# Kernel optimization log

Hardware: AMD Instinct MI355X
Metric: run time of the kernel (lower is better)

The kernel has to match this reference:

```python
import jax, jax.numpy as jnp
import numpy as np
import math

B, S = 2, 2048
DIM_MODEL = 2048
NUM_Q_HEADS = 16
GROUP_SIZE = 4
NUM_KV_HEADS = NUM_Q_HEADS // GROUP_SIZE
DIM_K = 128
RMS_EPS = 1e-6
ROPE_BASE = 10000.0


def setup_inputs() -> dict:
    key = jax.random.key(0)
    ks = jax.random.split(key, 8)
    x = jax.random.normal(ks[0], (B, S, DIM_MODEL), dtype=jnp.float32)
    mask = jnp.tril(jnp.ones((S, S), dtype=bool))  # causal
    # Linear weights stored as [in, out] so y = x @ W (bias=False everywhere)
    sd = 1.0 / math.sqrt(DIM_MODEL)
    Wq = jax.random.uniform(ks[1], (DIM_MODEL, DIM_K * NUM_Q_HEADS), jnp.float32, -sd, sd)
    Wk = jax.random.uniform(ks[2], (DIM_MODEL, DIM_K * NUM_KV_HEADS), jnp.float32, -sd, sd)
    Wv = jax.random.uniform(ks[3], (DIM_MODEL, DIM_K * NUM_KV_HEADS), jnp.float32, -sd, sd)
    sf = 1.0 / math.sqrt(DIM_K * NUM_Q_HEADS)
    Wfc = jax.random.uniform(ks[4], (DIM_K * NUM_Q_HEADS, DIM_MODEL), jnp.float32, -sf, sf)
    q_gamma = jnp.ones((DIM_K,), dtype=jnp.float32)
    k_gamma = jnp.ones((DIM_K,), dtype=jnp.float32)
    return {"x": x, "mask": mask, "Wq": Wq, "Wk": Wk, "Wv": Wv,
            "Wfc": Wfc, "q_gamma": q_gamma, "k_gamma": k_gamma}


def _rope(t):
    # t: [B, H, S, D], rotate-half RoPE
    d = t.shape[-1]
    half = d // 2
    inv_freq = 1.0 / (ROPE_BASE ** (jnp.arange(half, dtype=jnp.float32) / half))
    pos = jnp.arange(t.shape[2], dtype=jnp.float32)
    ang = pos[:, None] * inv_freq[None, :]            # [S, half]
    cos, sin = jnp.cos(ang), jnp.sin(ang)              # [S, half]
    t1, t2 = t[..., :half], t[..., half:]
    return jnp.concatenate([t1 * cos - t2 * sin, t2 * cos + t1 * sin], axis=-1)


def _rmsnorm(t, gamma):
    ms = jnp.mean(t * t, axis=-1, keepdims=True)
    return t * jax.lax.rsqrt(ms + RMS_EPS) * gamma


def reference(x, mask, Wq, Wk, Wv, Wfc, q_gamma, k_gamma):
    b, s, _ = x.shape
    q = (x @ Wq).reshape(b, s, NUM_Q_HEADS, DIM_K).transpose(0, 2, 1, 3)   # [B,Hq,S,D]
    k = (x @ Wk).reshape(b, s, NUM_KV_HEADS, DIM_K).transpose(0, 2, 1, 3)  # [B,Hkv,S,D]
    v = (x @ Wv).reshape(b, s, NUM_KV_HEADS, DIM_K).transpose(0, 2, 1, 3)
    q = _rmsnorm(_rope(q), q_gamma)
    k = _rmsnorm(_rope(k), k_gamma)
    q = q.reshape(b, NUM_KV_HEADS, GROUP_SIZE, s, DIM_K)                    # [B,Hkv,G,S,D]
    scores = jnp.einsum('bhgqd,bhkd->bhgqk', q, k) / math.sqrt(DIM_K)      # [B,Hkv,G,S,S]
    scores = jnp.where(mask, scores, -jnp.inf)
    attn = jax.nn.softmax(scores, axis=-1)  # dropout is identity in eval
    out = jnp.einsum('bhgqk,bhkd->bhgqd', attn, v)                          # [B,Hkv,G,S,D]
    out = out.reshape(b, NUM_Q_HEADS, s, DIM_K).transpose(0, 2, 1, 3)
    out = out.reshape(b, s, NUM_Q_HEADS * DIM_K) @ Wfc                      # [B,S,DM]
    return out
```

## Files before the change

kernel.cpp:

```cpp
#include <hip/hip_runtime.h>
#include <hip/hip_bf16.h>

typedef __attribute__((ext_vector_type(8))) short bf16x8;
typedef __attribute__((ext_vector_type(4))) short bf16x4;
typedef __attribute__((ext_vector_type(4))) float f32x4;

#define S_LEN 2048
#define DMODEL 2048
#define NQH 16
#define NKVH 4
#define DK 128

__device__ __forceinline__ float b2f(short u) {
  union { unsigned int i; float f; } x;
  x.i = ((unsigned int)(unsigned short)u) << 16;
  return x.f;
}
__device__ __forceinline__ short f2b(float f) {
  union { float f; unsigned int i; } x; x.f = f;
  unsigned int r = (x.i + 0x7fffu + ((x.i >> 16) & 1u)) >> 16;
  return (short)r;
}
__device__ __forceinline__ unsigned int cvtpk(float a, float b) {
  unsigned int r;
  asm("v_cvt_pk_bf16_f32 %0, %1, %2" : "=v"(r) : "v"(a), "v"(b));
  return r;
}
__device__ __forceinline__ f32x4 mfma16(bf16x8 a, bf16x8 b, f32x4 c) {
  return __builtin_amdgcn_mfma_f32_16x16x32_bf16(a, b, c, 0, 0, 0);
}
__device__ __forceinline__ void async16(short* lds, const short* g) {
  __builtin_amdgcn_global_load_lds(
      (const __attribute__((address_space(1))) unsigned int*)(const void*)g,
      (__attribute__((address_space(3))) unsigned int*)(void*)lds, 16, 0, 0);
}

__global__ void f32_to_bf16(const float* __restrict__ in, short* __restrict__ out, int n4) {
  int i = blockIdx.x * blockDim.x + threadIdx.x;
  if (i >= n4) return;
  float4 v = ((const float4*)in)[i];
  bf16x4 o;
  o[0] = f2b(v.x); o[1] = f2b(v.y); o[2] = f2b(v.z); o[3] = f2b(v.w);
  ((bf16x4*)out)[i] = o;
}

__global__ void rope_table(float* __restrict__ rt) {
  int i = blockIdx.x * blockDim.x + threadIdx.x;
  int s = i >> 6, d = i & 63;
  float ang = (float)s * __expf((float)d * -0.14391157f);
  float c, sn;
  __sincosf(ang, &sn, &c);
  rt[s * 128 + d] = c;
  rt[s * 128 + 64 + d] = sn;
}

__global__ void transpose_f2b(const float* __restrict__ in, short* __restrict__ out,
                              int R, int C) {
  __shared__ short t[32][33];
  int c0 = blockIdx.x * 32, r0 = blockIdx.y * 32;
  int tx = threadIdx.x, ty = threadIdx.y;
#pragma unroll
  for (int i = 0; i < 32; i += 8)
    t[ty + i][tx] = f2b(in[(size_t)(r0 + ty + i) * C + c0 + tx]);
  __syncthreads();
#pragma unroll
  for (int i = 0; i < 32; i += 8)
    out[(size_t)(c0 + ty + i) * R + r0 + tx] = t[tx][ty + i];
}

template <int NT, int VW>
__device__ __forceinline__ void kcore256(const short* __restrict__ Ab,
                                         const short* __restrict__ Bb,
                                         short* sm, f32x4 (&acc)[8][NT], int tid) {
  const int K = 2048;
  const int lane = tid & 63, w = tid >> 6;
  const int wm2 = w >> 2, wn4 = w & 3;
  const int l15 = lane & 15, lg = lane >> 4;
  constexpr int ABUF = 8192;
  constexpr int BBUF = NT * 2048;
  constexpr int BUFSZ = ABUF + BBUF;

  const int sr = lane >> 2, sc = lane & 3;
  const int ar0 = w * 16 + sr, ar1 = ar0 + 128;
  const short* gA0 = Ab + (size_t)ar0 * K + ((sc ^ (ar0 & 3)) * 8);
  const short* gA1 = Ab + (size_t)ar1 * K + ((sc ^ (ar1 & 3)) * 8);
  const short* gB0 = Bb + (size_t)ar0 * K + ((sc ^ (ar0 & 3)) * 8);
  const short* gB1 = Bb + (size_t)ar1 * K + ((sc ^ (ar1 & 3)) * 8);
  const int dA0 = (w * 16) * 32, dA1 = dA0 + 128 * 32;
  const int dB0 = ABUF + dA0, dB1 = ABUF + dA1;

  int aoff[8], boff[NT];
#pragma unroll
  for (int mt = 0; mt < 8; ++mt) {
    const int row = wm2 * 128 + mt * 16 + l15;
    aoff[mt] = row * 32 + ((lg * 8) ^ ((row & 3) << 3));
  }
#pragma unroll
  for (int nt = 0; nt < NT; ++nt) {
    const int row = wn4 * (NT * 16) + nt * 16 + l15;
    boff[nt] = ABUF + row * 32 + ((lg * 8) ^ ((row & 3) << 3));
  }

  auto stageA = [&](int buf, int t) {
    short* d = sm + buf * BUFSZ;
    const int o = t * 32;
    async16(d + dA0, gA0 + o);
    async16(d + dA1, gA1 + o);
  };
  auto stageB = [&](int buf, int t) {
    short* d = sm + buf * BUFSZ;
    const int o = t * 32;
    async16(d + dB0, gB0 + o);
    if constexpr (NT == 4) async16(d + dB1, gB1 + o);
  };
  auto tilebody = [&](int buf, int sbuf, int st, bool dostage) {
    const short* bc = sm + buf * BUFSZ;
    if (dostage) stageA(sbuf, st);
    bf16x8 bfr[NT], af[4];
#pragma unroll
    for (int nt = 0; nt < NT; ++nt) bfr[nt] = *(const bf16x8*)(bc + boff[nt]);
#pragma unroll
    for (int mt = 0; mt < 4; ++mt) af[mt] = *(const bf16x8*)(bc + aoff[mt]);
    __builtin_amdgcn_s_setprio(1);
#pragma unroll
    for (int mt = 0; mt < 4; ++mt)
#pragma unroll
      for (int nt = 0; nt < NT; ++nt)
        acc[mt][nt] = mfma16(af[mt], bfr[nt], acc[mt][nt]);
    __builtin_amdgcn_s_setprio(0);
    if (dostage) stageB(sbuf, st);
#pragma unroll
    for (int mt = 0; mt < 4; ++mt) af[mt] = *(const bf16x8*)(bc + aoff[4 + mt]);
    __builtin_amdgcn_s_setprio(1);
#pragma unroll
    for (int mt = 0; mt < 4; ++mt)
#pragma unroll
      for (int nt = 0; nt < NT; ++nt)
        acc[4 + mt][nt] = mfma16(af[mt], bfr[nt], acc[4 + mt][nt]);
    __builtin_amdgcn_s_setprio(0);
  };

  stageA(0, 0); stageB(0, 0);
  stageA(1, 1); stageB(1, 1);
  int cur = 0, nx2 = 2;
#pragma unroll 1
  for (int t = 0; t < 63; ++t) {
    __builtin_amdgcn_sched_barrier(0);
    if constexpr (VW == 4)
      asm volatile("s_waitcnt vmcnt(4)" ::: "memory");
    else
      asm volatile("s_waitcnt vmcnt(3)" ::: "memory");
    __builtin_amdgcn_s_barrier();
    __builtin_amdgcn_sched_barrier(0);
    tilebody(cur, nx2, t + 2, t < 62);
    cur = (cur == 2) ? 0 : cur + 1;
    nx2 = (nx2 == 2) ? 0 : nx2 + 1;
  }
  __builtin_amdgcn_sched_barrier(0);
  asm volatile("s_waitcnt vmcnt(0)" ::: "memory");
  __builtin_amdgcn_s_barrier();
  __builtin_amdgcn_sched_barrier(0);
  tilebody(cur, 0, 0, false);
}

__global__ __launch_bounds__(512) void gemm_qkv(const short* __restrict__ A,
                                                const short* __restrict__ WT,
                                                short* __restrict__ Qr,
                                                short* __restrict__ Kr,
                                                short* __restrict__ Vtr,
                                                const float* __restrict__ qg,
                                                const float* __restrict__ kg,
                                                const float* __restrict__ ropeT) {
  __shared__ __align__(16) short smem[49152];
  const int flat = blockIdx.x;
  const int xcd = flat & 7, idx = flat >> 3;
  const int mb = (xcd >> 1) * 4 + (idx & 3);
  const int nb = (xcd & 1) * 6 + (idx >> 2);
  const int tid = threadIdx.x;

  f32x4 acc[8][4] = {};
  kcore256<4, 4>(A + (size_t)mb * 256 * 2048, WT + (size_t)nb * 256 * 2048,
                 smem, acc, tid);

  const int lane = tid & 63, w = tid >> 6, wm2 = w >> 2, wn4 = w & 3;
  const int l15 = lane & 15, lg = lane >> 4;
  const int b = mb >> 3;
  short* Cs = smem;
  constexpr int CL = 264;

  for (int ph = 0; ph < 2; ++ph) {
    __syncthreads();
    if (wm2 == ph) {
#pragma unroll
      for (int mt = 0; mt < 8; ++mt)
#pragma unroll
        for (int nt = 0; nt < 4; ++nt)
#pragma unroll
          for (int rr = 0; rr < 4; ++rr)
            Cs[(mt * 16 + lg * 4 + rr) * CL + wn4 * 64 + nt * 16 + l15] =
                f2b(acc[mt][nt][rr]);
    }
    __syncthreads();
    const int srowg = mb * 256 + ph * 128;
    if (nb < 10) {
      const bool isQ = nb < 8;
      const int r = tid >> 2, quad = tid & 3;
      const int head = quad >> 1, half = quad & 1;
      const int s = (srowg + r) & 2047;
      const float* rt = ropeT + (size_t)s * 128;
      const short* crow = Cs + r * CL + head * 128;
      const float* gamma = isQ ? qg : kg;
      float ss = 0.f;
      bf16x8 ov[8];
#pragma unroll
      for (int j = 0; j < 8; ++j) {
        bf16x8 t1v = *(const bf16x8*)(crow + j * 8);
        bf16x8 t2v = *(const bf16x8*)(crow + 64 + j * 8);
        float4 c0 = *(const float4*)(rt + j * 8);
        float4 c1 = *(const float4*)(rt + j * 8 + 4);
        float4 s0 = *(const float4*)(rt + 64 + j * 8);
        float4 s1 = *(const float4*)(rt + 64 + j * 8 + 4);
        float cc[8] = {c0.x, c0.y, c0.z, c0.w, c1.x, c1.y, c1.z, c1.w};
        float sn[8] = {s0.x, s0.y, s0.z, s0.w, s1.x, s1.y, s1.z, s1.w};
#pragma unroll
        for (int i = 0; i < 8; ++i) {
          float t1 = b2f(t1v[i]), t2 = b2f(t2v[i]);
          float o = half ? (t2 * cc[i] + t1 * sn[i]) : (t1 * cc[i] - t2 * sn[i]);
          ss += o * o;
          ov[j][i] = f2b(o);
        }
      }
      ss += __shfl_xor(ss, 1);
      float inv = rsqrtf(ss * (1.0f / 128.0f) + 1e-6f);
      if (isQ) inv *= (0.08838834764831845f * 1.4426950408889634f);
      const int NH = isQ ? NQH : NKVH;
      const int hg = isQ ? (nb * 2 + head) : ((nb - 8) * 2 + head);
      short* outp = isQ ? Qr : Kr;
      short* ob = outp + ((size_t)(b * NH + hg) * S_LEN + s) * DK + half * 64;
#pragma unroll
      for (int j = 0; j < 8; ++j) {
        float4 g0 = *(const float4*)(gamma + half * 64 + j * 8);
        float4 g1 = *(const float4*)(gamma + half * 64 + j * 8 + 4);
        float gg[8] = {g0.x, g0.y, g0.z, g0.w, g1.x, g1.y, g1.z, g1.w};
        bf16x8 vv;
#pragma unroll
        for (int i = 0; i < 8; ++i) vv[i] = f2b(b2f(ov[j][i]) * inv * gg[i]);
        *(bf16x8*)(ob + j * 8) = vv;
      }
    } else {
      const int hd = tid >> 7;
      const int head = hd >> 1, sh = hd & 1;
      const int d = tid & 127;
      const int hg = (nb - 10) * 2 + head;
      const int sbase = (srowg & 2047) + sh * 64;
      short* ob = Vtr + ((size_t)(b * NKVH + hg) * DK + d) * S_LEN + sbase;
      const short* cc = Cs + head * 128 + d;
      for (int i0 = 0; i0 < 64; i0 += 8) {
        bf16x8 v;
#pragma unroll
        for (int j = 0; j < 8; ++j) {
          const int p = i0 + j;
          const int sl = sh * 64 + 16 * (p & 3) + (p >> 2);
          v[j] = cc[sl * CL];
        }
        *(bf16x8*)(ob + i0) = v;
      }
    }
  }
}

__global__ __launch_bounds__(512) void gemm_out(const short* __restrict__ A,
                                                const short* __restrict__ BT,
                                                float* __restrict__ outf) {
  __shared__ __align__(16) short smem[36864];
  const int flat = blockIdx.x;
  const int xcd = flat & 7, idx = flat >> 3;
  const int mb = (xcd >> 1) * 4 + (idx & 3);
  const int nb = (xcd & 1) * 8 + (idx >> 2);
  const int tid = threadIdx.x;

  f32x4 acc[8][2] = {};
  kcore256<2, 3>(A + (size_t)mb * 256 * 2048, BT + (size_t)nb * 128 * 2048,
                 smem, acc, tid);

  const int lane = tid & 63, w = tid >> 6, wm2 = w >> 2, wn4 = w & 3;
  const int l15 = lane & 15, lg = lane >> 4;
#pragma unroll
  for (int mt = 0; mt < 8; ++mt) {
    const int row = mb * 256 + wm2 * 128 + mt * 16 + lg * 4;
#pragma unroll
    for (int nt = 0; nt < 2; ++nt) {
      const int col = nb * 128 + wn4 * 32 + nt * 16 + l15;
#pragma unroll
      for (int r = 0; r < 4; ++r)
        outf[(size_t)(row + r) * DMODEL + col] = acc[mt][nt][r];
    }
  }
}

__device__ __forceinline__ void stage_kv(const short* __restrict__ Kb,
                                         const short* __restrict__ Vb, int kb,
                                         short* Ks, short* Vs, int w, int lane) {
#pragma unroll
  for (int i = 0; i < 4; ++i) {
    const int c = 4 * w + i;
    const int krow = c * 4 + (lane >> 4);
    const int kcol = (((lane & 15) * 16) ^ ((krow & 7) << 4)) >> 1;
    async16(Ks + c * 512, Kb + (size_t)(kb + krow) * DK + kcol);
    const int vrow = c * 8 + (lane >> 3);
    const int vcol = (((lane & 7) * 16) ^ ((vrow & 7) << 4)) >> 1;
    async16(Vs + c * 512, Vb + (size_t)vrow * S_LEN + kb + vcol);
  }
}

__device__ __forceinline__ void sm_pv(f32x4* sc, float* lsum, f32x4* acco,
                                      const short* Vc, short* Pw, int q0, bool diag,
                                      int kb, int l15, int lg) {
  if (diag) {
#pragma unroll
    for (int nt = 0; nt < 4; ++nt) {
      const int k = kb + nt * 16 + l15;
#pragma unroll
      for (int r = 0; r < 4; ++r)
        if (k > q0 + lg * 4 + r) sc[nt][r] = -1e30f;
    }
  }
#pragma unroll
  for (int r = 0; r < 4; ++r) {
    const float p0 = exp2f(sc[0][r]);
    const float p1 = exp2f(sc[1][r]);
    const float p2 = exp2f(sc[2][r]);
    const float p3 = exp2f(sc[3][r]);
    lsum[r] += (p0 + p1) + (p2 + p3);
    uint2 dv;
    dv.x = cvtpk(p0, p1);
    dv.y = cvtpk(p2, p3);
    *(uint2*)(Pw + (lg * 4 + r) * 72 + l15 * 4) = dv;
  }
#pragma unroll
  for (int kk = 0; kk < 2; ++kk) {
    bf16x8 ap = *(const bf16x8*)(Pw + l15 * 72 + kk * 32 + lg * 8);
#pragma unroll
    for (int dt = 0; dt < 8; ++dt) {
      const int vrow = dt * 16 + l15;
      bf16x8 bv = *(const bf16x8*)(Vc + vrow * 64 +
                                   (((kk * 64 + lg * 16) ^ ((vrow & 7) << 4)) >> 1));
      acco[dt] = mfma16(ap, bv, acco[dt]);
    }
  }
}

__device__ __forceinline__ void attn_writeout(f32x4* acco, float* lsum,
                                              short* __restrict__ AO, int b, int qh,
                                              int q0, int l15, int lg) {
  float ls[4];
#pragma unroll
  for (int r = 0; r < 4; ++r) {
    float t = lsum[r];
    t += __shfl_xor(t, 1);
    t += __shfl_xor(t, 2);
    t += __shfl_xor(t, 4);
    t += __shfl_xor(t, 8);
    ls[r] = 1.0f / t;
  }
  short* ob = AO + (size_t)(b * S_LEN + q0) * (NQH * DK) + qh * DK;
#pragma unroll
  for (int dt = 0; dt < 8; ++dt)
#pragma unroll
    for (int r = 0; r < 4; ++r)
      ob[(size_t)(lg * 4 + r) * (NQH * DK) + dt * 16 + l15] = f2b(acco[dt][r] * ls[r]);
}

__global__ __launch_bounds__(256, 2) void attn_kernel(const short* __restrict__ Qr,
                                                      const short* __restrict__ Kr,
                                                      const short* __restrict__ Vt,
                                                      short* __restrict__ AO) {
  const int flat = blockIdx.x;
  const int nw = (flat & 7) * 64 + (flat >> 3);
  const int qtA = nw & 15;
  const int bh = nw >> 4;
  const int qtB = 31 - qtA;
  const int b = bh >> 4, qh = bh & 15;
  const int kvh = qh >> 2;
  const short* Qb = Qr + (size_t)bh * S_LEN * DK;
  const short* Kb = Kr + (size_t)(b * NKVH + kvh) * S_LEN * DK;
  const short* Vb = Vt + (size_t)(b * NKVH + kvh) * DK * S_LEN;
  const int tid = threadIdx.x, lane = tid & 63, w = tid >> 6;
  const int l15 = lane & 15, lg = lane >> 4;

  __shared__ __align__(16) short KV[4][64 * 128];
  __shared__ __align__(16) short P[4][16][72];
  short* Pw = &P[w][0][0];

  const int q0A = qtA * 64 + w * 16, q0B = qtB * 64 + w * 16;
  bf16x8 aqA[4], aqB[4];
#pragma unroll
  for (int kk = 0; kk < 4; ++kk) {
    aqA[kk] = *(const bf16x8*)(Qb + (size_t)(q0A + l15) * DK + kk * 32 + lg * 8);
    aqB[kk] = *(const bf16x8*)(Qb + (size_t)(q0B + l15) * DK + kk * 32 + lg * 8);
  }

  f32x4 accoA[8] = {}, accoB[8] = {};
  float lsA[4] = {0.f, 0.f, 0.f, 0.f}, lsB[4] = {0.f, 0.f, 0.f, 0.f};

  short* Kcur = KV[0]; short* Vcur = KV[1];
  short* Knxt = KV[2]; short* Vnxt = KV[3];

  stage_kv(Kb, Vb, 0, Kcur, Vcur, w, lane);
  asm volatile("s_waitcnt vmcnt(0)" ::: "memory");
  __syncthreads();

  for (int kt = 0; kt <= qtB; ++kt) {
    const int kb = kt * 64;
    if (kt < qtB) stage_kv(Kb, Vb, kb + 64, Knxt, Vnxt, w, lane);

    if (kt <= qtA) {
      f32x4 scB[4] = {}, scA[4] = {};
#pragma unroll
      for (int kk = 0; kk < 4; ++kk)
#pragma unroll
        for (int nt = 0; nt < 4; ++nt) {
          const int krow = nt * 16 + l15;
          bf16x8 bk = *(const bf16x8*)(Kcur + krow * 128 +
                                       (((kk * 64 + lg * 16) ^ ((krow & 7) << 4)) >> 1));
          scB[nt] = mfma16(aqB[kk], bk, scB[nt]);
          scA[nt] = mfma16(aqA[kk], bk, scA[nt]);
        }
      sm_pv(scB, lsB, accoB, Vcur, Pw, q0B, false, kb, l15, lg);
      sm_pv(scA, lsA, accoA, Vcur, Pw, q0A, kt == qtA, kb, l15, lg);
    } else {
      f32x4 scB[4] = {};
#pragma unroll
      for (int kk = 0; kk < 4; ++kk)
#pragma unroll
        for (int nt = 0; nt < 4; ++nt) {
          const int krow = nt * 16 + l15;
          bf16x8 bk = *(const bf16x8*)(Kcur + krow * 128 +
                                       (((kk * 64 + lg * 16) ^ ((krow & 7) << 4)) >> 1));
          scB[nt] = mfma16(aqB[kk], bk, scB[nt]);
        }
      sm_pv(scB, lsB, accoB, Vcur, Pw, q0B, kt == qtB, kb, l15, lg);
    }

    asm volatile("s_waitcnt vmcnt(0)" ::: "memory");
    __syncthreads();
    short* t;
    t = Kcur; Kcur = Knxt; Knxt = t;
    t = Vcur; Vcur = Vnxt; Vnxt = t;
  }

  attn_writeout(accoB, lsB, AO, b, qh, q0B, l15, lg);
  attn_writeout(accoA, lsA, AO, b, qh, q0A, l15, lg);
}

extern "C" void kernel_launch(void* const* d_in, const int* in_sizes, int n_in,
                              void* d_out, int out_size, void* d_ws, size_t ws_size,
                              hipStream_t stream) {
  const float* x = (const float*)d_in[0];
  const float* Wq = (const float*)d_in[2];
  const float* Wk = (const float*)d_in[3];
  const float* Wv = (const float*)d_in[4];
  const float* Wfc = (const float*)d_in[5];
  const float* qg = (const float*)d_in[6];
  const float* kg = (const float*)d_in[7];

  short* ws = (short*)d_ws;
  short* xb = ws;
  short* WqkvT = xb + (size_t)4096 * 2048;
  short* WqT = WqkvT;
  short* WkT = WqT + (size_t)2048 * 2048;
  short* WvT = WkT + (size_t)512 * 2048;
  short* WfcT = WvT + (size_t)512 * 2048;
  short* Qr = WfcT + (size_t)2048 * 2048;
  short* Kr = Qr + (size_t)32 * 2048 * 128;
  short* Vt = Kr + (size_t)8 * 2048 * 128;
  float* ropeT = (float*)(Vt + (size_t)8 * 128 * 2048);
  short* AO = xb;

  f32_to_bf16<<<(4096 * 2048 / 4 + 255) / 256, 256, 0, stream>>>(x, xb, 4096 * 2048 / 4);
  rope_table<<<(2048 * 64 + 255) / 256, 256, 0, stream>>>(ropeT);

  dim3 tb(32, 8);
  transpose_f2b<<<dim3(2048 / 32, 2048 / 32), tb, 0, stream>>>(Wq, WqT, 2048, 2048);
  transpose_f2b<<<dim3(512 / 32, 2048 / 32), tb, 0, stream>>>(Wk, WkT, 2048, 512);
  transpose_f2b<<<dim3(512 / 32, 2048 / 32), tb, 0, stream>>>(Wv, WvT, 2048, 512);
  transpose_f2b<<<dim3(2048 / 32, 2048 / 32), tb, 0, stream>>>(Wfc, WfcT, 2048, 2048);

  gemm_qkv<<<192, 512, 0, stream>>>(xb, WqkvT, Qr, Kr, Vt, qg, kg, ropeT);

  attn_kernel<<<512, 256, 0, stream>>>(Qr, Kr, Vt, AO);

  gemm_out<<<256, 512, 0, stream>>>(AO, WfcT, (float*)d_out);
}
```

Baseline: 216.9 us.

## Shrink QKV GEMM tile to 256x128, double grid, change LDS swizzle

The QKV projection GEMM drops from 256x256 tiles (192 blocks) to 256x128 tiles (384 blocks), reusing the same 2-wide N core as the output GEMM. This gives better coverage of the 256 CUs and a smaller LDS footprint, at the cost of reloading A tiles twice as often. The epilogue now handles one head per block in a single pass, and the global-to-LDS staging layout and XOR swizzle are changed (row>>1 based) for both GEMMs. Launch bounds now request 4 waves per SIMD.

```diff
diff --git a/kernel.cpp b/kernel.cpp
--- a/kernel.cpp
+++ b/kernel.cpp
@@ -68,37 +68,36 @@
     out[(size_t)(c0 + ty + i) * R + r0 + tx] = t[tx][ty + i];
 }
 
-template <int NT, int VW>
 __device__ __forceinline__ void kcore256(const short* __restrict__ Ab,
                                          const short* __restrict__ Bb,
-                                         short* sm, f32x4 (&acc)[8][NT], int tid) {
+                                         short* sm, f32x4 (&acc)[8][2], int tid) {
   const int K = 2048;
   const int lane = tid & 63, w = tid >> 6;
   const int wm2 = w >> 2, wn4 = w & 3;
   const int l15 = lane & 15, lg = lane >> 4;
   constexpr int ABUF = 8192;
-  constexpr int BBUF = NT * 2048;
+  constexpr int BBUF = 4096;
   constexpr int BUFSZ = ABUF + BBUF;
 
   const int sr = lane >> 2, sc = lane & 3;
-  const int ar0 = w * 16 + sr, ar1 = ar0 + 128;
-  const short* gA0 = Ab + (size_t)ar0 * K + ((sc ^ (ar0 & 3)) * 8);
-  const short* gA1 = Ab + (size_t)ar1 * K + ((sc ^ (ar1 & 3)) * 8);
-  const short* gB0 = Bb + (size_t)ar0 * K + ((sc ^ (ar0 & 3)) * 8);
-  const short* gB1 = Bb + (size_t)ar1 * K + ((sc ^ (ar1 & 3)) * 8);
-  const int dA0 = (w * 16) * 32, dA1 = dA0 + 128 * 32;
-  const int dB0 = ABUF + dA0, dB1 = ABUF + dA1;
-
-  int aoff[8], boff[NT];
+  const int arow0 = w * 32 + sr, arow1 = arow0 + 16;
+  const int brow = w * 16 + sr;
+  const short* gA0 = Ab + (size_t)arow0 * K + ((sc ^ ((arow0 >> 1) & 3)) * 8);
+  const short* gA1 = Ab + (size_t)arow1 * K + ((sc ^ ((arow1 >> 1) & 3)) * 8);
+  const short* gB0 = Bb + (size_t)brow * K + ((sc ^ ((brow >> 1) & 3)) * 8);
+  const int dA0 = (w * 32) * 32, dA1 = dA0 + 16 * 32;
+  const int dB0 = ABUF + (w * 16) * 32;
+
+  int aoff[8], boff[2];
 #pragma unroll
   for (int mt = 0; mt < 8; ++mt) {
     const int row = wm2 * 128 + mt * 16 + l15;
-    aoff[mt] = row * 32 + ((lg * 8) ^ ((row & 3) << 3));
-  }
-#pragma unroll
-  for (int nt = 0; nt < NT; ++nt) {
-    const int row = wn4 * (NT * 16) + nt * 16 + l15;
-    boff[nt] = ABUF + row * 32 + ((lg * 8) ^ ((row & 3) << 3));
+    aoff[mt] = row * 32 + ((lg * 8) ^ (((row >> 1) & 3) * 8));
+  }
+#pragma unroll
+  for (int nt = 0; nt < 2; ++nt) {
+    const int row = wn4 * 32 + nt * 16 + l15;
+    boff[nt] = ABUF + row * 32 + ((lg * 8) ^ (((row >> 1) & 3) * 8));
   }
 
   auto stageA = [&](int buf, int t) {
@@ -109,23 +108,21 @@
   };
   auto stageB = [&](int buf, int t) {
     short* d = sm + buf * BUFSZ;
-    const int o = t * 32;
-    async16(d + dB0, gB0 + o);
-    if constexpr (NT == 4) async16(d + dB1, gB1 + o);
+    async16(d + dB0, gB0 + t * 32);
   };
   auto tilebody = [&](int buf, int sbuf, int st, bool dostage) {
     const short* bc = sm + buf * BUFSZ;
     if (dostage) stageA(sbuf, st);
-    bf16x8 bfr[NT], af[4];
-#pragma unroll
-    for (int nt = 0; nt < NT; ++nt) bfr[nt] = *(const bf16x8*)(bc + boff[nt]);
+    bf16x8 bfr[2], af[4];
+#pragma unroll
+    for (int nt = 0; nt < 2; ++nt) bfr[nt] = *(const bf16x8*)(bc + boff[nt]);
 #pragma unroll
     for (int mt = 0; mt < 4; ++mt) af[mt] = *(const bf16x8*)(bc + aoff[mt]);
     __builtin_amdgcn_s_setprio(1);
 #pragma unroll
     for (int mt = 0; mt < 4; ++mt)
 #pragma unroll
-      for (int nt = 0; nt < NT; ++nt)
+      for (int nt = 0; nt < 2; ++nt)
         acc[mt][nt] = mfma16(af[mt], bfr[nt], acc[mt][nt]);
     __builtin_amdgcn_s_setprio(0);
     if (dostage) stageB(sbuf, st);
@@ -135,7 +132,7 @@
 #pragma unroll
     for (int mt = 0; mt < 4; ++mt)
 #pragma unroll
-      for (int nt = 0; nt < NT; ++nt)
+      for (int nt = 0; nt < 2; ++nt)
         acc[4 + mt][nt] = mfma16(af[mt], bfr[nt], acc[4 + mt][nt]);
     __builtin_amdgcn_s_setprio(0);
   };
@@ -146,10 +143,7 @@
 #pragma unroll 1
   for (int t = 0; t < 63; ++t) {
     __builtin_amdgcn_sched_barrier(0);
-    if constexpr (VW == 4)
-      asm volatile("s_waitcnt vmcnt(4)" ::: "memory");
-    else
-      asm volatile("s_waitcnt vmcnt(3)" ::: "memory");
+    asm volatile("s_waitcnt vmcnt(3)" ::: "memory");
     __builtin_amdgcn_s_barrier();
     __builtin_amdgcn_sched_barrier(0);
     tilebody(cur, nx2, t + 2, t < 62);
@@ -163,115 +157,110 @@
   tilebody(cur, 0, 0, false);
 }
 
-__global__ __launch_bounds__(512) void gemm_qkv(const short* __restrict__ A,
-                                                const short* __restrict__ WT,
-                                                short* __restrict__ Qr,
-                                                short* __restrict__ Kr,
-                                                short* __restrict__ Vtr,
-                                                const float* __restrict__ qg,
-                                                const float* __restrict__ kg,
-                                                const float* __restrict__ ropeT) {
-  __shared__ __align__(16) short smem[49152];
+__global__ __launch_bounds__(512, 4) void gemm_qkv(const short* __restrict__ A,
+                                                   const short* __restrict__ WT,
+                                                   short* __restrict__ Qr,
+                                                   short* __restrict__ Kr,
+                                                   short* __restrict__ Vtr,
+                                                   const float* __restrict__ qg,
+                                                   const float* __restrict__ kg,
+                                                   const float* __restrict__ ropeT) {
+  __shared__ __align__(16) short smem[36864];
   const int flat = blockIdx.x;
   const int xcd = flat & 7, idx = flat >> 3;
   const int mb = (xcd >> 1) * 4 + (idx & 3);
-  const int nb = (xcd & 1) * 6 + (idx >> 2);
+  const int nb = (xcd & 1) * 12 + (idx >> 2);
   const int tid = threadIdx.x;
 
-  f32x4 acc[8][4] = {};
-  kcore256<4, 4>(A + (size_t)mb * 256 * 2048, WT + (size_t)nb * 256 * 2048,
-                 smem, acc, tid);
+  f32x4 acc[8][2] = {};
+  kcore256(A + (size_t)mb * 256 * 2048, WT + (size_t)nb * 128 * 2048,
+           smem, acc, tid);
 
   const int lane = tid & 63, w = tid >> 6, wm2 = w >> 2, wn4 = w & 3;
   const int l15 = lane & 15, lg = lane >> 4;
   const int b = mb >> 3;
   short* Cs = smem;
-  constexpr int CL = 264;
-
-  for (int ph = 0; ph < 2; ++ph) {
-    __syncthreads();
-    if (wm2 == ph) {
-#pragma unroll
-      for (int mt = 0; mt < 8; ++mt)
-#pragma unroll
-        for (int nt = 0; nt < 4; ++nt)
-#pragma unroll
-          for (int rr = 0; rr < 4; ++rr)
-            Cs[(mt * 16 + lg * 4 + rr) * CL + wn4 * 64 + nt * 16 + l15] =
-                f2b(acc[mt][nt][rr]);
-    }
-    __syncthreads();
-    const int srowg = mb * 256 + ph * 128;
-    if (nb < 10) {
-      const bool isQ = nb < 8;
-      const int r = tid >> 2, quad = tid & 3;
-      const int head = quad >> 1, half = quad & 1;
-      const int s = (srowg + r) & 2047;
-      const float* rt = ropeT + (size_t)s * 128;
-      const short* crow = Cs + r * CL + head * 128;
-      const float* gamma = isQ ? qg : kg;
-      float ss = 0.f;
-      bf16x8 ov[8];
+  constexpr int CL = 136;
+
+  __syncthreads();
+#pragma unroll
+  for (int mt = 0; mt < 8; ++mt)
+#pragma unroll
+    for (int nt = 0; nt < 2; ++nt)
+#pragma unroll
+      for (int rr = 0; rr < 4; ++rr)
+        Cs[(wm2 * 128 + mt * 16 + lg * 4 + rr) * CL + wn4 * 32 + nt * 16 + l15] =
+            f2b(acc[mt][nt][rr]);
+  __syncthreads();
+
+  const int srow0 = mb * 256;
+  if (nb < 20) {
+    const bool isQ = nb < 16;
+    const int h = isQ ? nb : nb - 16;
+    const float* gamma = isQ ? qg : kg;
+    const int r = tid >> 1, half = tid & 1;
+    const int s = (srow0 + r) & 2047;
+    const float* rt = ropeT + (size_t)s * 128;
+    const short* crow = Cs + r * CL;
+    float ss = 0.f;
+    bf16x8 ov[8];
+#pragma unroll
+    for (int j = 0; j < 8; ++j) {
+      bf16x8 t1v = *(const bf16x8*)(crow + j * 8);
+      bf16x8 t2v = *(const bf16x8*)(crow + 64 + j * 8);
+      float4 c0 = *(const float4*)(rt + j * 8);
+      float4 c1 = *(const float4*)(rt + j * 8 + 4);
+      float4 s0 = *(const float4*)(rt + 64 + j * 8);
+      float4 s1 = *(const float4*)(rt + 64 + j * 8 + 4);
+      float cc[8] = {c0.x, c0.y, c0.z, c0.w, c1.x, c1.y, c1.z, c1.w};
+      float sn[8] = {s0.x, s0.y, s0.z, s0.w, s1.x, s1.y, s1.z, s1.w};
+#pragma unroll
+      for (int i = 0; i < 8; ++i) {
+        float t1 = b2f(t1v[i]), t2 = b2f(t2v[i]);
+        float o = half ? (t2 * cc[i] + t1 * sn[i]) : (t1 * cc[i] - t2 * sn[i]);
+        ss += o * o;
+        ov[j][i] = f2b(o);
+      }
+    }
+    ss += __shfl_xor(ss, 1);
+    float inv = rsqrtf(ss * (1.0f / 128.0f) + 1e-6f);
+    if (isQ) inv *= (0.08838834764831845f * 1.4426950408889634f);
+    const int NH = isQ ? NQH : NKVH;
+    short* outp = isQ ? Qr : Kr;
+    short* ob = outp + ((size_t)(b * NH + h) * S_LEN + s) * DK + half * 64;
+#pragma unroll
+    for (int j = 0; j < 8; ++j) {
+      float4 g0 = *(const float4*)(gamma + half * 64 + j * 8);
+      float4 g1 = *(const float4*)(gamma + half * 64 + j * 8 + 4);
+      float gg[8] = {g0.x, g0.y, g0.z, g0.w, g1.x, g1.y, g1.z, g1.w};
+      bf16x8 vv;
+#pragma unroll
+      for (int i = 0; i < 8; ++i) vv[i] = f2b(b2f(ov[j][i]) * inv * gg[i]);
+      *(bf16x8*)(ob + j * 8) = vv;
+    }
+  } else {
+    const int h = nb - 20;
+    const int d = tid & 127;
+    const int sh = tid >> 7;
+    const int sbase = (srow0 & 2047) + sh * 64;
+    short* ob = Vtr + ((size_t)(b * NKVH + h) * DK + d) * S_LEN + sbase;
+    const short* cc = Cs + d;
+    for (int i0 = 0; i0 < 64; i0 += 8) {
+      bf16x8 v;
 #pragma unroll
       for (int j = 0; j < 8; ++j) {
-        bf16x8 t1v = *(const bf16x8*)(crow + j * 8);
-        bf16x8 t2v = *(const bf16x8*)(crow + 64 + j * 8);
-        float4 c0 = *(const float4*)(rt + j * 8);
-        float4 c1 = *(const float4*)(rt + j * 8 + 4);
-        float4 s0 = *(const float4*)(rt + 64 + j * 8);
-        float4 s1 = *(const float4*)(rt + 64 + j * 8 + 4);
-        float cc[8] = {c0.x, c0.y, c0.z, c0.w, c1.x, c1.y, c1.z, c1.w};
-        float sn[8] = {s0.x, s0.y, s0.z, s0.w, s1.x, s1.y, s1.z, s1.w};
-#pragma unroll
-        for (int i = 0; i < 8; ++i) {
-          float t1 = b2f(t1v[i]), t2 = b2f(t2v[i]);
-          float o = half ? (t2 * cc[i] + t1 * sn[i]) : (t1 * cc[i] - t2 * sn[i]);
-          ss += o * o;
-          ov[j][i] = f2b(o);
-        }
+        const int p = i0 + j;
+        const int sl = sh * 64 + 16 * (p & 3) + (p >> 2);
+        v[j] = cc[sl * CL];
       }
-      ss += __shfl_xor(ss, 1);
-      float inv = rsqrtf(ss * (1.0f / 128.0f) + 1e-6f);
-      if (isQ) inv *= (0.08838834764831845f * 1.4426950408889634f);
-      const int NH = isQ ? NQH : NKVH;
-      const int hg = isQ ? (nb * 2 + head) : ((nb - 8) * 2 + head);
-      short* outp = isQ ? Qr : Kr;
-      short* ob = outp + ((size_t)(b * NH + hg) * S_LEN + s) * DK + half * 64;
-#pragma unroll
-      for (int j = 0; j < 8; ++j) {
-        float4 g0 = *(const float4*)(gamma + half * 64 + j * 8);
-        float4 g1 = *(const float4*)(gamma + half * 64 + j * 8 + 4);
-        float gg[8] = {g0.x, g0.y, g0.z, g0.w, g1.x, g1.y, g1.z, g1.w};
-        bf16x8 vv;
-#pragma unroll
-        for (int i = 0; i < 8; ++i) vv[i] = f2b(b2f(ov[j][i]) * inv * gg[i]);
-        *(bf16x8*)(ob + j * 8) = vv;
-      }
-    } else {
-      const int hd = tid >> 7;
-      const int head = hd >> 1, sh = hd & 1;
-      const int d = tid & 127;
-      const int hg = (nb - 10) * 2 + head;
-      const int sbase = (srowg & 2047) + sh * 64;
-      short* ob = Vtr + ((size_t)(b * NKVH + hg) * DK + d) * S_LEN + sbase;
-      const short* cc = Cs + head * 128 + d;
-      for (int i0 = 0; i0 < 64; i0 += 8) {
-        bf16x8 v;
-#pragma unroll
-        for (int j = 0; j < 8; ++j) {
-          const int p = i0 + j;
-          const int sl = sh * 64 + 16 * (p & 3) + (p >> 2);
-          v[j] = cc[sl * CL];
-        }
-        *(bf16x8*)(ob + i0) = v;
-      }
-    }
-  }
-}
-
-__global__ __launch_bounds__(512) void gemm_out(const short* __restrict__ A,
-                                                const short* __restrict__ BT,
-                                                float* __restrict__ outf) {
+      *(bf16x8*)(ob + i0) = v;
+    }
+  }
+}
+
+__global__ __launch_bounds__(512, 4) void gemm_out(const short* __restrict__ A,
+                                                   const short* __restrict__ BT,
+                                                   float* __restrict__ outf) {
   __shared__ __align__(16) short smem[36864];
   const int flat = blockIdx.x;
   const int xcd = flat & 7, idx = flat >> 3;
@@ -280,8 +269,8 @@
   const int tid = threadIdx.x;
 
   f32x4 acc[8][2] = {};
-  kcore256<2, 3>(A + (size_t)mb * 256 * 2048, BT + (size_t)nb * 128 * 2048,
-                 smem, acc, tid);
+  kcore256(A + (size_t)mb * 256 * 2048, BT + (size_t)nb * 128 * 2048,
+           smem, acc, tid);
 
   const int lane = tid & 63, w = tid >> 6, wm2 = w >> 2, wn4 = w & 3;
   const int l15 = lane & 15, lg = lane >> 4;
@@ -486,7 +475,7 @@
   transpose_f2b<<<dim3(512 / 32, 2048 / 32), tb, 0, stream>>>(Wv, WvT, 2048, 512);
   transpose_f2b<<<dim3(2048 / 32, 2048 / 32), tb, 0, stream>>>(Wfc, WfcT, 2048, 2048);
 
-  gemm_qkv<<<192, 512, 0, stream>>>(xb, WqkvT, Qr, Kr, Vt, qg, kg, ropeT);
+  gemm_qkv<<<384, 512, 0, stream>>>(xb, WqkvT, Qr, Kr, Vt, qg, kg, ropeT);
 
   attn_kernel<<<512, 256, 0, stream>>>(Qr, Kr, Vt, AO);
 
```

Result: faster. 206.1 us (-5.0%).
